# Optimization experiments

Hardware: AMD Instinct MI355X
Metric: run time of the kernel (lower is better)

The kernel has to match this reference:

```python
import jax, jax.numpy as jnp
import numpy as np

K, D = 8, 32          # num_heads, node_out_dim
KD = K * D            # 256
NEG = 0.2             # LeakyReLU negative slope
N, E = 100000, 300000
DIN, DREL = 128, 64


def setup_inputs() -> dict:
    key = jax.random.key(0)
    ks = iter(jax.random.split(key, 64))
    def nrm(shape, scale):
        return jax.random.normal(next(ks), shape, jnp.float32) * scale
    inp = {}
    # per-relation target-node features feats[(s,e,d)] : (N_d, d_in)
    for nm in ["feat_ui", "feat_iu", "feat_ii", "feat_ii_rev"]:
        inp[nm] = nrm((N, DIN), 1.0)
    # relation input features (d_rel,)
    for nm in ["r_ui", "r_iu", "r_ii", "r_ii_rev"]:
        inp[nm] = nrm((DREL,), 1.0)
    # fc_node per ntype (no bias), shared for src/dst roles
    inp["W_user"] = nrm((DIN, KD), 0.05)
    inp["W_item"] = nrm((DIN, KD), 0.05)
    # fc_rel per etype (no bias): d_rel -> 2*K*d
    for nm in ["Wrel_ui", "Wrel_iu", "Wrel_ii", "Wrel_ii_rev"]:
        inp[nm] = nrm((DREL, 2 * KD), 0.05)
    # cross-relation attention vectors (K, d)
    for nm in ["attn_ui", "attn_iu", "attn_ii", "attn_ii_rev"]:
        inp[nm] = nrm((K, D), 0.1)
    # residual fc per ntype (with bias) and residual gate scalar
    inp["Wres_user"] = nrm((DIN, KD), 0.05); inp["bres_user"] = nrm((KD,), 0.02)
    inp["Wres_item"] = nrm((DIN, KD), 0.05); inp["bres_item"] = nrm((KD,), 0.02)
    inp["a_user"] = jax.random.uniform(next(ks), (1,), jnp.float32)
    inp["a_item"] = jax.random.uniform(next(ks), (1,), jnp.float32)
    # fc_upd per etype (with bias): d_rel -> K*rel_out
    for nm in ["ui", "iu", "ii", "ii_rev"]:
        inp["Wupd_" + nm] = nrm((DREL, KD), 0.05)
        inp["bupd_" + nm] = nrm((KD,), 0.02)
    # edge lists per relation
    for nm in ["ui", "iu", "ii", "ii_rev"]:
        inp["src_" + nm] = jax.random.randint(next(ks), (E,), 0, N, jnp.int32)
        inp["dst_" + nm] = jax.random.randint(next(ks), (E,), 0, N, jnp.int32)
    return inp


def _conv(fsrc_in, fdst_in, Ws, Wd, Wrel, rfeat, src, dst):
    """RelationGraphConv: GAT-style attention over one bipartite relation."""
    n_dst = fdst_in.shape[0]
    fs = (fsrc_in @ Ws).reshape(-1, K, D)          # (Ns, K, D)
    fd = (fdst_in @ Wd).reshape(-1, K, D)          # (Nd, K, D)
    attn = (rfeat @ Wrel).reshape(K, 2 * D)        # (K, 2D)
    el = (fs * attn[:, :D]).sum(-1)                # (Ns, K)
    er = (fd * attn[:, D:]).sum(-1)                # (Nd, K)
    e = jax.nn.leaky_relu(el[src] + er[dst], NEG)  # (E, K)
    # edge softmax per destination node
    m = jax.ops.segment_max(e, dst, num_segments=n_dst)
    ex = jnp.exp(e - m[dst])
    s = jax.ops.segment_sum(ex, dst, num_segments=n_dst)
    a = ex / s[dst]                                # (E, K)
    msg = fs[src] * a[:, :, None]                  # (E, K, D)
    out = jax.ops.segment_sum(msg, dst, num_segments=n_dst)
    return jax.nn.relu(out.reshape(n_dst, KD))     # activation = relu


def _crossing(stacked, rel_attn):
    """RelationCrossing over stacked per-relation dst reps (R, N, K*D)."""
    R, Nn = stacked.shape[0], stacked.shape[1]
    f = stacked.reshape(R, Nn, K, D)
    sc = (rel_attn * f).sum(-1, keepdims=True)             # (R, N, K, 1)
    sc = jax.nn.softmax(jax.nn.leaky_relu(sc, NEG), axis=0)
    return (sc * f).sum(0).reshape(Nn, KD)


def reference(feat_ui, feat_iu, feat_ii, feat_ii_rev,
              r_ui, r_iu, r_ii, r_ii_rev,
              W_user, W_item,
              Wrel_ui, Wrel_iu, Wrel_ii, Wrel_ii_rev,
              attn_ui, attn_iu, attn_ii, attn_ii_rev,
              Wres_user, bres_user, Wres_item, bres_item,
              a_user, a_item,
              Wupd_ui, bupd_ui, Wupd_iu, bupd_iu,
              Wupd_ii, bupd_ii, Wupd_ii_rev, bupd_ii_rev,
              src_ui, dst_ui, src_iu, dst_iu,
              src_ii, dst_ii, src_ii_rev, dst_ii_rev):
    # relation convs; src feats come from the reverse relation's dict entry
    h_ui = _conv(feat_iu, feat_ui, W_user, W_item, Wrel_ui, r_ui, src_ui, dst_ui)
    h_iu = _conv(feat_ui, feat_iu, W_item, W_user, Wrel_iu, r_iu, src_iu, dst_iu)
    h_ii = _conv(feat_ii_rev, feat_ii, W_item, W_item, Wrel_ii, r_ii, src_ii, dst_ii)
    h_iir = _conv(feat_ii, feat_ii_rev, W_item, W_item, Wrel_ii_rev, r_ii_rev, src_ii_rev, dst_ii_rev)

    # gated residual per dtype
    def resid(h, fdst, Wres, bres, a):
        al = jax.nn.sigmoid(a)
        return al * h + (1.0 - al) * (fdst @ Wres + bres)

    h_ui = resid(h_ui, feat_ui, Wres_item, bres_item, a_item)
    h_iu = resid(h_iu, feat_iu, Wres_user, bres_user, a_user)
    h_ii = resid(h_ii, feat_ii, Wres_item, bres_item, a_item)
    h_iir = resid(h_iir, feat_ii_rev, Wres_item, bres_item, a_item)

    # cross-relation fusion: dtype item has relations [ui, ii, ii_rev]; user has [iu]
    item_stack = jnp.stack([h_ui, h_ii, h_iir], axis=0)
    out_ui = _crossing(item_stack, attn_ui)
    out_iu = h_iu  # num_rel == 1 -> identity
    out_ii = _crossing(item_stack, attn_ii)
    out_iir = _crossing(item_stack, attn_ii_rev)

    # relation feature update
    ro_ui = r_ui @ Wupd_ui + bupd_ui
    ro_iu = r_iu @ Wupd_iu + bupd_iu
    ro_ii = r_ii @ Wupd_ii + bupd_ii
    ro_iir = r_ii_rev @ Wupd_ii_rev + bupd_ii_rev
    return (out_ui, out_iu, out_ii, out_iir, ro_ui, ro_iu, ro_ii, ro_iir)
```

## Files before the change

### kernel.cpp

```cpp
#include <hip/hip_runtime.h>
#include <hip/hip_bf16.h>
#include <math.h>

#define NEG_SLOPE 0.2f
#define LOG2E 1.4426950408889634f

using bf16x8 = __attribute__((ext_vector_type(8))) short;
using f32x4  = __attribute__((ext_vector_type(4))) float;
using u16x8  = __attribute__((ext_vector_type(8))) unsigned short;
using u16x4  = __attribute__((ext_vector_type(4))) unsigned short;

__device__ __forceinline__ float lrelu(float x) { return x > 0.f ? x : NEG_SLOPE * x; }
__device__ __forceinline__ float dot4(float4 a, float4 b) {
    return a.x * b.x + a.y * b.y + a.z * b.z + a.w * b.w;
}
__device__ __forceinline__ unsigned short f2b(float x) {
    union { float f; unsigned u; } v; v.f = x;
    unsigned r = v.u + 0x7fff + ((v.u >> 16) & 1);
    return (unsigned short)(r >> 16);
}
__device__ __forceinline__ float b2f(unsigned short b) {
    union { unsigned u; float f; } v; v.u = ((unsigned)b) << 16;
    return v.f;
}
__device__ __forceinline__ float4 load4b(const unsigned short* p) {
    u16x4 u = *reinterpret_cast<const u16x4*>(p);
    return make_float4(b2f(u[0]), b2f(u[1]), b2f(u[2]), b2f(u[3]));
}
__device__ __forceinline__ bf16x8 cvt8(float4 a0, float4 a1) {
    union { u16x8 u; bf16x8 b; } c;
    c.u[0] = f2b(a0.x); c.u[1] = f2b(a0.y); c.u[2] = f2b(a0.z); c.u[3] = f2b(a0.w);
    c.u[4] = f2b(a1.x); c.u[5] = f2b(a1.y); c.u[6] = f2b(a1.z); c.u[7] = f2b(a1.w);
    return c.b;
}

struct PackArgs {
    const float* W1[4];
    const float* W2[4];
    const float* wvA[4];
    const float* wvB[4];
    unsigned short* Bp[4];
};

__global__ __launch_bounds__(256)
void pack_b_k(PackArgs pa)
{
    const int r = blockIdx.y;
    const int nb = blockIdx.x;
    const int ks = threadIdx.x >> 6;
    const int lane = threadIdx.x & 63;
    const int n = nb * 16 + (lane & 15);
    const int k0 = ks * 32 + (lane >> 4) * 8;
    u16x8 u;
    if (n < 512) {
        const float* Wsrc = (n < 256) ? (pa.W1[r] + n) : (pa.W2[r] + (n - 256));
        #pragma unroll
        for (int e = 0; e < 8; ++e) u[e] = f2b(Wsrc[(size_t)(k0 + e) * 256]);
    } else {
        const int h = (n - 512) & 7;
        const bool isEr = (n >= 520);
        const float* wv = isEr ? (pa.wvB[r] + h * 64 + 32) : (pa.wvA[r] + h * 64);
        const float* Wc = pa.W1[r] + h * 32;
        #pragma unroll
        for (int e = 0; e < 8; ++e) {
            const size_t k = (size_t)(k0 + e);
            float s = 0.f;
            #pragma unroll 8
            for (int d = 0; d < 32; ++d) s = fmaf(Wc[k * 256 + d], wv[d], s);
            u[e] = f2b(s);
        }
    }
    const size_t gid = (size_t)((nb * 4 + ks) * 64 + lane);
    *reinterpret_cast<u16x8*>(pa.Bp[r] + gid * 8) = u;
}

struct GemmArgs {
    const float* A[4];
    const unsigned short* Bp[4];
    const float* bres[4];
    unsigned short* pool[4];
    unsigned short* resid[4];
    float* elOut[4];
    float* erOut[4];
};

__global__ __launch_bounds__(256)
void mfma_gemm_k(GemmArgs ga, int Nrows)
{
    __shared__ __align__(16) char smem[65536];
    unsigned short* slab = (unsigned short*)smem;
    char* bounce = smem + 32768;
    const int rsel = blockIdx.y;
    const int t = threadIdx.x;
    const int wv = t >> 6, lane = t & 63;
    const int l15 = lane & 15, lg = lane >> 4;
    const int nloc = wv * 16 + l15;
    const int m0 = blockIdx.x * 64;
    const int node = m0 + nloc;
    const bool valid = node < Nrows;
    const int nc = valid ? node : (Nrows - 1);

    const float* __restrict__ A = ga.A[rsel];
    const unsigned short* __restrict__ Bp = ga.Bp[rsel];
    const float* __restrict__ bres = ga.bres[rsel];

    bf16x8 bfr[4];
    #pragma unroll
    for (int ks = 0; ks < 4; ++ks) {
        const float* p = A + (size_t)nc * 128 + ks * 32 + lg * 8;
        float4 a0 = *reinterpret_cast<const float4*>(p);
        float4 a1 = *reinterpret_cast<const float4*>(p + 4);
        bfr[ks] = cvt8(a0, a1);
    }

    const int swz = (nloc & 7) << 4;

    u16x8 sreg[8];
    #pragma unroll
    for (int j = 0; j < 8; ++j)
        sreg[j] = *reinterpret_cast<const u16x8*>(Bp + (size_t)(j * 256 + t) * 8);

    u16x8 snext;

    #pragma unroll
    for (int p = 0; p < 4; ++p) {
        #pragma unroll
        for (int j = 0; j < 8; ++j)
            *reinterpret_cast<u16x8*>(slab + (size_t)(j * 256 + t) * 8) = sreg[j];
        __syncthreads();
        if (p < 3) {
            const unsigned short* src = Bp + (size_t)(p + 1) * 16384;
            #pragma unroll
            for (int j = 0; j < 8; ++j)
                sreg[j] = *reinterpret_cast<const u16x8*>(src + (size_t)(j * 256 + t) * 8);
        } else {
            snext = *reinterpret_cast<const u16x8*>(Bp + (size_t)65536 + (size_t)t * 8);
        }
        const bool isPool = (p < 2);
        #pragma unroll
        for (int i = 0; i < 8; ++i) {
            const int ni = p * 8 + i;
            f32x4 acc = (f32x4){0.f, 0.f, 0.f, 0.f};
            #pragma unroll
            for (int ks = 0; ks < 4; ++ks) {
                bf16x8 wf = *reinterpret_cast<const bf16x8*>(
                    slab + (size_t)((i * 4 + ks) * 64 + lane) * 8);
                acc = __builtin_amdgcn_mfma_f32_16x16x32_bf16(wf, bfr[ks], acc, 0, 0, 0);
            }
            const int cni = isPool ? ni : (ni - 16);
            u16x4 o;
            if (isPool) {
                o[0] = f2b(acc[0]); o[1] = f2b(acc[1]);
                o[2] = f2b(acc[2]); o[3] = f2b(acc[3]);
            } else {
                float4 bv = *reinterpret_cast<const float4*>(bres + cni * 16 + lg * 4);
                o[0] = f2b(acc[0] + bv.x); o[1] = f2b(acc[1] + bv.y);
                o[2] = f2b(acc[2] + bv.z); o[3] = f2b(acc[3] + bv.w);
            }
            *reinterpret_cast<u16x4*>(bounce + nloc * 512 + ((cni * 32 + lg * 8) ^ swz)) = o;
        }
        __syncthreads();
        if (p == 1) {
            unsigned short* __restrict__ dst = ga.pool[rsel];
            #pragma unroll
            for (int i = 0; i < 8; ++i) {
                const int chunk = i * 256 + t;
                const int row = chunk >> 5;
                const int c16 = chunk & 31;
                const int byte = row * 512 + ((c16 * 16) ^ ((row & 7) << 4));
                u16x8 v = *reinterpret_cast<const u16x8*>(bounce + byte);
                if (m0 + row < Nrows)
                    *reinterpret_cast<u16x8*>(dst + (size_t)(m0 + row) * 256 + c16 * 8) = v;
            }
            __syncthreads();
        }
    }
    *reinterpret_cast<u16x8*>(slab + (size_t)t * 8) = snext;
    {
        unsigned short* __restrict__ dst = ga.resid[rsel];
        #pragma unroll
        for (int i = 0; i < 8; ++i) {
            const int chunk = i * 256 + t;
            const int row = chunk >> 5;
            const int c16 = chunk & 31;
            const int byte = row * 512 + ((c16 * 16) ^ ((row & 7) << 4));
            u16x8 v = *reinterpret_cast<const u16x8*>(bounce + byte);
            if (m0 + row < Nrows)
                *reinterpret_cast<u16x8*>(dst + (size_t)(m0 + row) * 256 + c16 * 8) = v;
        }
    }
    __syncthreads();
    {
        f32x4 acc = (f32x4){0.f, 0.f, 0.f, 0.f};
        #pragma unroll
        for (int ks = 0; ks < 4; ++ks) {
            bf16x8 wf = *reinterpret_cast<const bf16x8*>(
                slab + (size_t)(ks * 64 + lane) * 8);
            acc = __builtin_amdgcn_mfma_f32_16x16x32_bf16(wf, bfr[ks], acc, 0, 0, 0);
        }
        if (valid) {
            float4 v = make_float4(acc[0], acc[1], acc[2], acc[3]);
            if (lg < 2)
                *reinterpret_cast<float4*>(ga.elOut[rsel] + (size_t)node * 8 + lg * 4) = v;
            else
                *reinterpret_cast<float4*>(ga.erOut[rsel] + (size_t)node * 8 + (lg - 2) * 4) = v;
        }
    }
}

struct EdgePtrs {
    const int* src[4];
    const int* dst[4];
    int E[4];
    int csrOff[4];
};

__global__ __launch_bounds__(256)
void hist_k(EdgePtrs ep, int* __restrict__ counts4, int N)
{
    const int r = blockIdx.y;
    const int e = blockIdx.x * 256 + threadIdx.x;
    if (e < ep.E[r]) atomicAdd(counts4 + (size_t)r * N + ep.dst[r][e], 1);
}

__global__ __launch_bounds__(256)
void blksum_k(const int* __restrict__ counts4, int* __restrict__ blksum4, int N)
{
    const int r = blockIdx.y;
    const int* c = counts4 + (size_t)r * N;
    const int base = blockIdx.x * 1024 + threadIdx.x;
    int s = 0;
    #pragma unroll
    for (int i = 0; i < 4; ++i) { int idx = base + i * 256; if (idx < N) s += c[idx]; }
    __shared__ int sd[256];
    sd[threadIdx.x] = s; __syncthreads();
    for (int off = 128; off > 0; off >>= 1) {
        if (threadIdx.x < off) sd[threadIdx.x] += sd[threadIdx.x + off];
        __syncthreads();
    }
    if (threadIdx.x == 0) blksum4[r * 1024 + blockIdx.x] = sd[0];
}

__global__ __launch_bounds__(1024)
void scanblk_k(int* __restrict__ blksum4, int nbx)
{
    const int r = blockIdx.x;
    const int t = threadIdx.x;
    __shared__ int sd[1024];
    int v = (t < nbx) ? blksum4[r * 1024 + t] : 0;
    sd[t] = v; __syncthreads();
    for (int off = 1; off < 1024; off <<= 1) {
        int u = (t >= off) ? sd[t - off] : 0;
        __syncthreads();
        sd[t] += u;
        __syncthreads();
    }
    if (t < nbx) blksum4[r * 1024 + t] = sd[t] - v;
}

__global__ __launch_bounds__(256)
void cursor_k(const int* __restrict__ counts4, const int* __restrict__ blkoff4,
              int* __restrict__ cursor4, int N)
{
    const int r = blockIdx.y;
    const int* c = counts4 + (size_t)r * N;
    int* cur = cursor4 + (size_t)r * N;
    const int t = threadIdx.x;
    const int base = blockIdx.x * 1024 + t * 4;
    const int c0 = (base + 0 < N) ? c[base + 0] : 0;
    const int c1 = (base + 1 < N) ? c[base + 1] : 0;
    const int c2 = (base + 2 < N) ? c[base + 2] : 0;
    const int c3 = (base + 3 < N) ? c[base + 3] : 0;
    const int tsum = c0 + c1 + c2 + c3;
    __shared__ int sd[256];
    sd[t] = tsum; __syncthreads();
    for (int off = 1; off < 256; off <<= 1) {
        int u = (t >= off) ? sd[t - off] : 0;
        __syncthreads();
        sd[t] += u;
        __syncthreads();
    }
    int excl = sd[t] - tsum + blkoff4[r * 1024 + blockIdx.x];
    if (base + 0 < N) cur[base + 0] = excl;
    if (base + 1 < N) cur[base + 1] = excl + c0;
    if (base + 2 < N) cur[base + 2] = excl + c0 + c1;
    if (base + 3 < N) cur[base + 3] = excl + c0 + c1 + c2;
}

__global__ __launch_bounds__(256)
void scatter_k(EdgePtrs ep, int* __restrict__ cursor4, int* __restrict__ csr_src, int N)
{
    const int r = blockIdx.y;
    const int e = blockIdx.x * 256 + threadIdx.x;
    if (e < ep.E[r]) {
        const int d = ep.dst[r][e];
        const int pos = atomicAdd(cursor4 + (size_t)r * N + d, 1);
        csr_src[ep.csrOff[r] + pos] = ep.src[r][e];
    }
}

struct NodeArgs {
    const int* csr[4];
    const int* cursor[4];
    const int* counts[4];
    const float* el[4];
    const float* er[4];
    const unsigned short* pool[4];
    const unsigned short* resid[4];
};

__global__ __launch_bounds__(256)
void node_k(NodeArgs na,
            const float* __restrict__ attn_ui, const float* __restrict__ attn_ii,
            const float* __restrict__ attn_iir,
            const float* __restrict__ a_user, const float* __restrict__ a_item,
            float* __restrict__ out, int Nrows)
{
    const int lane = threadIdx.x & 63;
    const int n = blockIdx.x * 4 + (threadIdx.x >> 6);
    if (n >= Nrows) return;
    const int k = lane >> 3;

    int deg[4], endv[4];
    float erk[4];
    #pragma unroll
    for (int r = 0; r < 4; ++r) {
        deg[r]  = na.counts[r][n];
        endv[r] = na.cursor[r][n];
        erk[r]  = na.er[r][(size_t)n * 8 + k];
    }

    const float si = 1.f / (1.f + __expf(-a_item[0])), osi = 1.f - si;
    const float su = 1.f / (1.f + __expf(-a_user[0])), osu = 1.f - su;

    float4 fr[4];
    #pragma unroll
    for (int r = 0; r < 4; ++r) {
        const int d = deg[r];
        const int start = endv[r] - d;
        const int* __restrict__ csr = na.csr[r];
        const float* __restrict__ elr = na.el[r];
        const unsigned short* __restrict__ fs = na.pool[r];
        const float er_k = erk[r];
        float s = 0.f;
        float4 acc = make_float4(0.f, 0.f, 0.f, 0.f);
        for (int base = 0; base < d; base += 4) {
            const int m = d - base;
            int sidx[4];
            #pragma unroll
            for (int u = 0; u < 4; ++u)
                sidx[u] = csr[start + base + ((u < m) ? u : 0)];
            float ex[4];
            #pragma unroll
            for (int u = 0; u < 4; ++u) {
                const float x = elr[(size_t)sidx[u] * 8 + k] + er_k;
                const float e = __builtin_amdgcn_exp2f(fmaxf(x, NEG_SLOPE * x));
                ex[u] = (u < m) ? e : 0.f;
            }
            float4 pv[4];
            #pragma unroll
            for (int u = 0; u < 4; ++u)
                pv[u] = load4b(fs + (size_t)sidx[u] * 256 + lane * 4);
            #pragma unroll
            for (int u = 0; u < 4; ++u) {
                s += ex[u];
                acc.x = fmaf(pv[u].x, ex[u], acc.x);
                acc.y = fmaf(pv[u].y, ex[u], acc.y);
                acc.z = fmaf(pv[u].z, ex[u], acc.z);
                acc.w = fmaf(pv[u].w, ex[u], acc.w);
            }
        }
        const float inv = (d > 0) ? 1.f / s : 0.f;
        float4 R = load4b(na.resid[r] + (size_t)n * 256 + lane * 4);
        const float sg = (r == 1) ? su : si;
        const float og = (r == 1) ? osu : osi;
        fr[r].x = sg * fmaxf(acc.x * inv, 0.f) + og * R.x;
        fr[r].y = sg * fmaxf(acc.y * inv, 0.f) + og * R.y;
        fr[r].z = sg * fmaxf(acc.z * inv, 0.f) + og * R.z;
        fr[r].w = sg * fmaxf(acc.w * inv, 0.f) + og * R.w;
    }

    const float4 f0 = fr[0], f1 = fr[2], f2 = fr[3], fiu = fr[1];
    float4 w0 = *reinterpret_cast<const float4*>(attn_ui  + lane * 4);
    float4 w1 = *reinterpret_cast<const float4*>(attn_ii  + lane * 4);
    float4 w2 = *reinterpret_cast<const float4*>(attn_iir + lane * 4);

    float p[3][3];
    p[0][0] = dot4(w0, f0); p[0][1] = dot4(w0, f1); p[0][2] = dot4(w0, f2);
    p[1][0] = dot4(w1, f0); p[1][1] = dot4(w1, f1); p[1][2] = dot4(w1, f2);
    p[2][0] = dot4(w2, f0); p[2][1] = dot4(w2, f1); p[2][2] = dot4(w2, f2);
    #pragma unroll
    for (int x = 0; x < 3; ++x)
        #pragma unroll
        for (int r = 0; r < 3; ++r)
            #pragma unroll
            for (int m = 1; m < 8; m <<= 1)
                p[x][r] += __shfl_xor(p[x][r], m, 64);

    const size_t NK = (size_t)Nrows * 256;
    const size_t o = (size_t)n * 256 + lane * 4;
    const size_t xoff[3] = {0, 2 * NK, 3 * NK};
    #pragma unroll
    for (int x = 0; x < 3; ++x) {
        float a0 = lrelu(p[x][0]), a1 = lrelu(p[x][1]), a2 = lrelu(p[x][2]);
        float mx = fmaxf(a0, fmaxf(a1, a2));
        float e0 = __expf(a0 - mx), e1 = __expf(a1 - mx), e2 = __expf(a2 - mx);
        float inv = 1.f / (e0 + e1 + e2);
        e0 *= inv; e1 *= inv; e2 *= inv;
        float4 rr;
        rr.x = e0 * f0.x + e1 * f1.x + e2 * f2.x;
        rr.y = e0 * f0.y + e1 * f1.y + e2 * f2.y;
        rr.z = e0 * f0.z + e1 * f1.z + e2 * f2.z;
        rr.w = e0 * f0.w + e1 * f1.w + e2 * f2.w;
        *reinterpret_cast<float4*>(out + xoff[x] + o) = rr;
    }
    *reinterpret_cast<float4*>(out + NK + o) = fiu;
}

struct RelPtrs {
    const float* rf[4];
    const float* Wrel[4];
    const float* Wupd[4];
    const float* bupd[4];
};

__global__ __launch_bounds__(512)
void rel_k(RelPtrs P, float* __restrict__ wvec, float* __restrict__ ro)
{
    const int r = blockIdx.x;
    const int t = threadIdx.x;
    __shared__ float rfs[64];
    if (t < 64) rfs[t] = P.rf[r][t];
    __syncthreads();
    {
        const float* Wc = P.Wrel[r];
        float acc = 0.f;
        #pragma unroll 8
        for (int i = 0; i < 64; ++i) acc = fmaf(rfs[i], Wc[(size_t)i * 512 + t], acc);
        wvec[(size_t)r * 512 + t] = acc * LOG2E;
    }
    if (t < 256) {
        const float* Wc = P.Wupd[r];
        float acc = P.bupd[r][t];
        #pragma unroll 8
        for (int i = 0; i < 64; ++i) acc = fmaf(rfs[i], Wc[(size_t)i * 256 + t], acc);
        ro[(size_t)r * 256 + t] = acc;
    }
}

extern "C" void kernel_launch(void* const* d_in, const int* in_sizes, int n_in,
                              void* d_out, int out_size, void* d_ws, size_t ws_size,
                              hipStream_t stream)
{
    (void)n_in; (void)out_size; (void)ws_size;
    const float* feat_ui  = (const float*)d_in[0];
    const float* feat_iu  = (const float*)d_in[1];
    const float* feat_ii  = (const float*)d_in[2];
    const float* feat_iir = (const float*)d_in[3];
    const float* W_user   = (const float*)d_in[8];
    const float* W_item   = (const float*)d_in[9];
    const float* Wres_user = (const float*)d_in[18];
    const float* bres_user = (const float*)d_in[19];
    const float* Wres_item = (const float*)d_in[20];
    const float* bres_item = (const float*)d_in[21];
    const float* a_user = (const float*)d_in[22];
    const float* a_item = (const float*)d_in[23];
    const int N = in_sizes[0] / 128;
    const int Es[4] = {in_sizes[32], in_sizes[34], in_sizes[36], in_sizes[38]};
    int maxE = 0;
    for (int r = 0; r < 4; ++r) maxE = Es[r] > maxE ? Es[r] : maxE;

    const size_t NP = (size_t)N * 256;
    const size_t N8 = (size_t)N * 8;
    const size_t BPSZ = 33 * 4 * 64 * 8;

    unsigned short* us = (unsigned short*)d_ws;
    unsigned short* pool[4];
    unsigned short* resid[4];
    for (int r = 0; r < 4; ++r) pool[r]  = us + (size_t)r * NP;
    for (int r = 0; r < 4; ++r) resid[r] = us + (size_t)(4 + r) * NP;
    unsigned short* BpArr[4];
    for (int r = 0; r < 4; ++r) BpArr[r] = us + 8 * NP + (size_t)r * BPSZ;
    float* fl = (float*)(us + 8 * NP + 4 * BPSZ);
    float *el[4], *er[4];
    for (int r = 0; r < 4; ++r) { el[r] = fl + (size_t)(2 * r) * N8; er[r] = fl + (size_t)(2 * r + 1) * N8; }
    float* wvec = fl + 8 * N8;
    int* counts4 = (int*)(wvec + 4 * 512);
    int* cursor4 = counts4 + 4 * (size_t)N;
    int* blksum4 = cursor4 + 4 * (size_t)N;
    int* csr_src = blksum4 + 4 * 1024;
    float* out = (float*)d_out;

    EdgePtrs ep;
    {
        int off = 0;
        const int si[4] = {32, 34, 36, 38};
        for (int r = 0; r < 4; ++r) {
            ep.src[r] = (const int*)d_in[si[r]];
            ep.dst[r] = (const int*)d_in[si[r] + 1];
            ep.E[r] = Es[r];
            ep.csrOff[r] = off;
            off += Es[r];
        }
    }

    (void)hipMemsetAsync(counts4, 0, 4 * (size_t)N * sizeof(int), stream);

    RelPtrs rp;
    rp.rf[0]   = (const float*)d_in[4];  rp.rf[1]   = (const float*)d_in[5];
    rp.rf[2]   = (const float*)d_in[6];  rp.rf[3]   = (const float*)d_in[7];
    rp.Wrel[0] = (const float*)d_in[10]; rp.Wrel[1] = (const float*)d_in[11];
    rp.Wrel[2] = (const float*)d_in[12]; rp.Wrel[3] = (const float*)d_in[13];
    rp.Wupd[0] = (const float*)d_in[24]; rp.Wupd[1] = (const float*)d_in[26];
    rp.Wupd[2] = (const float*)d_in[28]; rp.Wupd[3] = (const float*)d_in[30];
    rp.bupd[0] = (const float*)d_in[25]; rp.bupd[1] = (const float*)d_in[27];
    rp.bupd[2] = (const float*)d_in[29]; rp.bupd[3] = (const float*)d_in[31];
    rel_k<<<dim3(4), dim3(512), 0, stream>>>(rp, wvec, out + 4 * NP);

    const int pair[4] = {1, 0, 3, 2};
    PackArgs pa;
    pa.W1[0] = W_user; pa.W2[0] = Wres_user;
    pa.W1[1] = W_item; pa.W2[1] = Wres_item;
    pa.W1[2] = W_item; pa.W2[2] = Wres_item;
    pa.W1[3] = W_item; pa.W2[3] = Wres_item;
    for (int r = 0; r < 4; ++r) {
        pa.wvA[r] = wvec + (size_t)r * 512;
        pa.wvB[r] = wvec + (size_t)pair[r] * 512;
        pa.Bp[r]  = BpArr[r];
    }
    pack_b_k<<<dim3(33, 4), 256, 0, stream>>>(pa);

    const int geb = (maxE + 255) / 256;
    const int nbx = (N + 1023) / 1024;
    hist_k<<<dim3(geb, 4), 256, 0, stream>>>(ep, counts4, N);
    blksum_k<<<dim3(nbx, 4), 256, 0, stream>>>(counts4, blksum4, N);
    scanblk_k<<<dim3(4), 1024, 0, stream>>>(blksum4, nbx);
    cursor_k<<<dim3(nbx, 4), 256, 0, stream>>>(counts4, blksum4, cursor4, N);
    scatter_k<<<dim3(geb, 4), 256, 0, stream>>>(ep, cursor4, csr_src, N);

    GemmArgs ga;
    ga.A[0] = feat_iu;  ga.bres[0] = bres_user;
    ga.A[1] = feat_ui;  ga.bres[1] = bres_item;
    ga.A[2] = feat_iir; ga.bres[2] = bres_item;
    ga.A[3] = feat_ii;  ga.bres[3] = bres_item;
    for (int r = 0; r < 4; ++r) {
        ga.Bp[r]    = BpArr[r];
        ga.pool[r]  = pool[r];
        ga.resid[r] = resid[pair[r]];
        ga.elOut[r] = el[r];
        ga.erOut[r] = er[pair[r]];
    }
    const int gb = (N + 63) / 64;
    mfma_gemm_k<<<dim3(gb, 4), 256, 0, stream>>>(ga, N);

    NodeArgs na;
    for (int r = 0; r < 4; ++r) {
        na.csr[r]    = csr_src + ep.csrOff[r];
        na.cursor[r] = cursor4 + (size_t)r * N;
        na.counts[r] = counts4 + (size_t)r * N;
        na.el[r]     = el[r];
        na.er[r]     = er[r];
        na.pool[r]   = pool[r];
        na.resid[r]  = resid[r];
    }
    const int nb4 = (N + 3) / 4;
    node_k<<<nb4, 256, 0, stream>>>(na,
                                    (const float*)d_in[14], (const float*)d_in[16],
                                    (const float*)d_in[17],
                                    a_user, a_item, out, N);
}
```

Baseline: 571.6 us.

## Halve GEMM bounce buffer and use 32-bit index math in node gather

The GEMM kernel now writes each 128-column quarter of the output to a half-size LDS bounce buffer and flushes it to global memory after every pass, rather than staging 256 columns before each flush. This cuts shared memory per block from 64KB to 48KB so more blocks can fit per CU, at the cost of more frequent, narrower global write phases. The node aggregation kernel switches gather address arithmetic from size_t to unsigned 32-bit to lower VALU and register cost, which relies on the offsets fitting in 32 bits.

```diff
diff --git a/kernel.cpp b/kernel.cpp
--- a/kernel.cpp
+++ b/kernel.cpp
@@ -87,7 +87,7 @@
 __global__ __launch_bounds__(256)
 void mfma_gemm_k(GemmArgs ga, int Nrows)
 {
-    __shared__ __align__(16) char smem[65536];
+    __shared__ __align__(16) char smem[49152];
     unsigned short* slab = (unsigned short*)smem;
     char* bounce = smem + 32768;
     const int rsel = blockIdx.y;
@@ -139,7 +139,6 @@
         const bool isPool = (p < 2);
         #pragma unroll
         for (int i = 0; i < 8; ++i) {
-            const int ni = p * 8 + i;
             f32x4 acc = (f32x4){0.f, 0.f, 0.f, 0.f};
             #pragma unroll
             for (int ks = 0; ks < 4; ++ks) {
@@ -147,48 +146,36 @@
                     slab + (size_t)((i * 4 + ks) * 64 + lane) * 8);
                 acc = __builtin_amdgcn_mfma_f32_16x16x32_bf16(wf, bfr[ks], acc, 0, 0, 0);
             }
-            const int cni = isPool ? ni : (ni - 16);
             u16x4 o;
             if (isPool) {
                 o[0] = f2b(acc[0]); o[1] = f2b(acc[1]);
                 o[2] = f2b(acc[2]); o[3] = f2b(acc[3]);
             } else {
-                float4 bv = *reinterpret_cast<const float4*>(bres + cni * 16 + lg * 4);
+                const int cb = (p - 2) * 128 + i * 16 + lg * 4;
+                float4 bv = *reinterpret_cast<const float4*>(bres + cb);
                 o[0] = f2b(acc[0] + bv.x); o[1] = f2b(acc[1] + bv.y);
                 o[2] = f2b(acc[2] + bv.z); o[3] = f2b(acc[3] + bv.w);
             }
-            *reinterpret_cast<u16x4*>(bounce + nloc * 512 + ((cni * 32 + lg * 8) ^ swz)) = o;
-        }
-        __syncthreads();
-        if (p == 1) {
-            unsigned short* __restrict__ dst = ga.pool[rsel];
-            #pragma unroll
-            for (int i = 0; i < 8; ++i) {
-                const int chunk = i * 256 + t;
-                const int row = chunk >> 5;
-                const int c16 = chunk & 31;
-                const int byte = row * 512 + ((c16 * 16) ^ ((row & 7) << 4));
+            *reinterpret_cast<u16x4*>(bounce + nloc * 256 + ((i * 32 + lg * 8) ^ swz)) = o;
+        }
+        __syncthreads();
+        {
+            unsigned short* __restrict__ dst = isPool ? ga.pool[rsel] : ga.resid[rsel];
+            const int colbase = (p & 1) * 128;
+            #pragma unroll
+            for (int it = 0; it < 4; ++it) {
+                const int chunk = it * 256 + t;
+                const int row = chunk >> 4;
+                const int c16 = chunk & 15;
+                const int byte = row * 256 + ((c16 * 16) ^ ((row & 7) << 4));
                 u16x8 v = *reinterpret_cast<const u16x8*>(bounce + byte);
                 if (m0 + row < Nrows)
-                    *reinterpret_cast<u16x8*>(dst + (size_t)(m0 + row) * 256 + c16 * 8) = v;
+                    *reinterpret_cast<u16x8*>(dst + (size_t)(m0 + row) * 256
+                                              + colbase + c16 * 8) = v;
             }
-            __syncthreads();
         }
     }
     *reinterpret_cast<u16x8*>(slab + (size_t)t * 8) = snext;
-    {
-        unsigned short* __restrict__ dst = ga.resid[rsel];
-        #pragma unroll
-        for (int i = 0; i < 8; ++i) {
-            const int chunk = i * 256 + t;
-            const int row = chunk >> 5;
-            const int c16 = chunk & 31;
-            const int byte = row * 512 + ((c16 * 16) ^ ((row & 7) << 4));
-            u16x8 v = *reinterpret_cast<const u16x8*>(bounce + byte);
-            if (m0 + row < Nrows)
-                *reinterpret_cast<u16x8*>(dst + (size_t)(m0 + row) * 256 + c16 * 8) = v;
-        }
-    }
     __syncthreads();
     {
         f32x4 acc = (f32x4){0.f, 0.f, 0.f, 0.f};
@@ -319,14 +306,16 @@
     const int lane = threadIdx.x & 63;
     const int n = blockIdx.x * 4 + (threadIdx.x >> 6);
     if (n >= Nrows) return;
-    const int k = lane >> 3;
-
-    int deg[4], endv[4];
+    const unsigned k = (unsigned)(lane >> 3);
+    const unsigned c4 = (unsigned)(lane * 4);
+
+    int deg[4], start[4];
     float erk[4];
     #pragma unroll
     for (int r = 0; r < 4; ++r) {
         deg[r]  = na.counts[r][n];
-        endv[r] = na.cursor[r][n];
+        const int endv = na.cursor[r][n];
+        start[r] = endv - deg[r];
         erk[r]  = na.er[r][(size_t)n * 8 + k];
     }
 
@@ -337,7 +326,7 @@
     #pragma unroll
     for (int r = 0; r < 4; ++r) {
         const int d = deg[r];
-        const int start = endv[r] - d;
+        const int st = start[r];
         const int* __restrict__ csr = na.csr[r];
         const float* __restrict__ elr = na.el[r];
         const unsigned short* __restrict__ fs = na.pool[r];
@@ -349,18 +338,18 @@
             int sidx[4];
             #pragma unroll
             for (int u = 0; u < 4; ++u)
-                sidx[u] = csr[start + base + ((u < m) ? u : 0)];
+                sidx[u] = csr[st + base + ((u < m) ? u : 0)];
             float ex[4];
             #pragma unroll
             for (int u = 0; u < 4; ++u) {
-                const float x = elr[(size_t)sidx[u] * 8 + k] + er_k;
+                const float x = elr[(unsigned)sidx[u] * 8u + k] + er_k;
                 const float e = __builtin_amdgcn_exp2f(fmaxf(x, NEG_SLOPE * x));
                 ex[u] = (u < m) ? e : 0.f;
             }
             float4 pv[4];
             #pragma unroll
             for (int u = 0; u < 4; ++u)
-                pv[u] = load4b(fs + (size_t)sidx[u] * 256 + lane * 4);
+                pv[u] = load4b(fs + (unsigned)sidx[u] * 256u + c4);
             #pragma unroll
             for (int u = 0; u < 4; ++u) {
                 s += ex[u];
@@ -371,7 +360,7 @@
             }
         }
         const float inv = (d > 0) ? 1.f / s : 0.f;
-        float4 R = load4b(na.resid[r] + (size_t)n * 256 + lane * 4);
+        float4 R = load4b(na.resid[r] + (unsigned)n * 256u + c4);
         const float sg = (r == 1) ? su : si;
         const float og = (r == 1) ? osu : osi;
         fr[r].x = sg * fmaxf(acc.x * inv, 0.f) + og * R.x;
```

Result: faster. 557.8 us, median of 2 (-2.4%).
